# Optimization experiments

Hardware: AMD Instinct MI355X
Metric: run time of the kernel (lower is better)

The kernel has to match this reference:

```python
import jax, jax.numpy as jnp
import numpy as np

ALPHA = 0.2  # LeakyReLU negative slope
NEG_INF = -9e15


def setup_inputs() -> dict:
    key = jax.random.key(0)
    k1, k2, k3, k4, k5 = jax.random.split(key, 5)
    B, N, D = 4, 4096, 256
    feat = jax.random.normal(k1, (B, N, D), dtype=jnp.float32)
    adj = jax.random.randint(k2, (B, N, N), 0, 2, dtype=jnp.int32)
    W = jax.random.normal(k3, (D, D), dtype=jnp.float32) * (1.414 / np.sqrt(D))
    a_1 = jax.random.normal(k4, (D, 1), dtype=jnp.float32) * 0.1
    a_2 = jax.random.normal(k5, (D, 1), dtype=jnp.float32) * 0.1
    return {"feat": feat, "adj": adj, "W": W, "a_1": a_1, "a_2": a_2}


def reference(feat, adj, W, a_1, a_2):
    # h: [B, N, D]
    h = jnp.matmul(feat, W)
    Ax = jnp.matmul(h, a_1)  # [B, N, 1]
    Ay = jnp.matmul(h, a_2)  # [B, N, 1]
    # logits[b, i, j] = Ax[b, j] + Ay[b, i]
    logits = jnp.swapaxes(Ax, 1, 2) + Ay  # [B, N, N]
    e = jax.nn.leaky_relu(logits, negative_slope=ALPHA)
    e = jnp.where(adj > 0, e, jnp.float32(NEG_INF))
    attention = jax.nn.softmax(e, axis=-1)  # dropout p=0.0 -> identity
    h_prime = jnp.matmul(attention, feat)  # [B, N, in_features]
    h_out = jnp.matmul(h_prime, W)  # [B, N, out_features]
    return jax.nn.elu(h_out)
```

## Files before the change

### kernel.cpp

```cpp
#include <hip/hip_runtime.h>

typedef __attribute__((ext_vector_type(8))) short short8;
typedef __attribute__((ext_vector_type(4))) float f32x4;
typedef __attribute__((ext_vector_type(4))) int i32x4;
typedef __attribute__((ext_vector_type(2))) unsigned u32x2;

#define LOG2E 1.44269504f

__device__ __forceinline__ short f2bf(float f) {
  unsigned u = __builtin_bit_cast(unsigned, f);
  u += 0x7fffu + ((u >> 16) & 1u);
  return (short)(u >> 16);
}

__global__ void gat_wvec(const float* __restrict__ W, const float* __restrict__ a1,
                         const float* __restrict__ a2, float* __restrict__ w1,
                         float* __restrict__ w2) {
  __shared__ float a1f[256], a2f[256];
  const int tid = threadIdx.x;
  a1f[tid] = a1[tid];
  a2f[tid] = a2[tid];
  __syncthreads();
  float s1 = 0.f, s2 = 0.f;
  const float4* wr = (const float4*)(W + (size_t)tid * 256);
  for (int d0 = 0; d0 < 64; ++d0) {
    float4 v = wr[d0];
    s1 += v.x * a1f[d0 * 4] + v.y * a1f[d0 * 4 + 1] + v.z * a1f[d0 * 4 + 2] + v.w * a1f[d0 * 4 + 3];
    s2 += v.x * a2f[d0 * 4] + v.y * a2f[d0 * 4 + 1] + v.z * a2f[d0 * 4 + 2] + v.w * a2f[d0 * 4 + 3];
  }
  w1[tid] = s1;
  w2[tid] = s2;
}

__global__ void packB(const float* __restrict__ src, short* __restrict__ dst, int F) {
  const int tid = threadIdx.x;
  const int f = blockIdx.x, b = blockIdx.y;
  const int g = tid >> 4, l15 = tid & 15;
  const float* s = src + ((size_t)b * F * 32 + f * 32) * 256 + g * 16 + l15;
  short* d = dst + (((size_t)(b * F + f) * 16 + g) * 64) * 8;
#pragma unroll
  for (int q = 0; q < 4; ++q) {
    short8 v;
#pragma unroll
    for (int j8 = 0; j8 < 8; ++j8) v[j8] = f2bf(s[(q * 8 + j8) * 256]);
    *(short8*)(d + (q * 16 + l15) * 8) = v;
  }
}

__global__ void gat_axay(const float* __restrict__ feat, const float* __restrict__ w1,
                         const float* __restrict__ w2, float* __restrict__ AxL,
                         float* __restrict__ AyL) {
  const int lane = threadIdx.x & 63;
  const int row = blockIdx.x * 4 + (threadIdx.x >> 6);
  float4 fv = *(const float4*)(feat + (size_t)row * 256 + lane * 4);
  const float4 w1v = *(const float4*)(w1 + lane * 4);
  const float4 w2v = *(const float4*)(w2 + lane * 4);
  float s1 = fv.x * w1v.x + fv.y * w1v.y + fv.z * w1v.z + fv.w * w1v.w;
  float s2 = fv.x * w2v.x + fv.y * w2v.y + fv.z * w2v.z + fv.w * w2v.w;
#pragma unroll
  for (int off = 32; off >= 1; off >>= 1) {
    s1 += __shfl_xor(s1, off);
    s2 += __shfl_xor(s2, off);
  }
  if (lane == 0) { AxL[row] = s1 * LOG2E; AyL[row] = s2 * LOG2E; }
}

__global__ void gat_max(const float* __restrict__ AxL, float* __restrict__ MbL) {
  __shared__ float red[256];
  const int b = blockIdx.x, tid = threadIdx.x;
  float m = -3.4e38f;
  for (int i = tid; i < 4096; i += 256) m = fmaxf(m, AxL[b * 4096 + i]);
  red[tid] = m;
  __syncthreads();
  for (int s = 128; s > 0; s >>= 1) {
    if (tid < s) red[tid] = fmaxf(red[tid], red[tid + s]);
    __syncthreads();
  }
  if (tid == 0) MbL[b] = red[0];
}

__global__ __launch_bounds__(512, 4) void gat_attn(
    const short* __restrict__ featB,
    const int* __restrict__ adj,
    const float* __restrict__ AxL, const float* __restrict__ AyL,
    const float* __restrict__ MbL,
    const short* __restrict__ WB,
    float* __restrict__ out)
{
  __shared__ short smem[16896];

  const int tid = threadIdx.x;
  const int blk = blockIdx.x;
  const int x = blk & 7;
  const int b = x >> 1;
  const int it = ((blk >> 3) << 1) | (x & 1);
  const int i0 = it << 5;
  const int scoff = (blk >> 3) & 15;

  const int lane = tid & 63;
  const int aw = tid >> 6;

  float aLk[4], ddk[4];
#pragma unroll
  for (int k = 0; k < 4; ++k) {
    float ayL = AyL[b * 4096 + i0 + aw * 4 + k];
    float sL = ayL + MbL[b];
    float mrL = fmaxf(sL, 0.2f * sL);
    aLk[k] = ayL - mrL;
    ddk[k] = -0.8f * mrL;
  }
  const int* adjr = adj + ((size_t)(b * 4096 + i0 + aw * 4)) * 4096 + lane * 4;
  const float4* axp = (const float4*)(AxL + b * 4096) + lane;

  const int w = aw;
  const int rowg = (w & 1) << 4;
  const int cgrp = (w >> 1) << 2;
  const int l15 = lane & 15;
  const int q = lane >> 4;

  f32x4 acc[4], lac;
  lac = (f32x4){0.f, 0.f, 0.f, 0.f};
#pragma unroll
  for (int j = 0; j < 4; ++j) acc[j] = (f32x4){0.f, 0.f, 0.f, 0.f};

  short8 ones;
#pragma unroll
  for (int j = 0; j < 8; ++j) ones[j] = (short)0x3F80;

  const short* fbb = featB + (size_t)b * 128 * 16 * 64 * 8 + lane * 8;

  i32x4 adv[4];
  float4 axv;
  {
    const int w0 = scoff;
#pragma unroll
    for (int k = 0; k < 4; ++k)
      adv[k] = __builtin_nontemporal_load((const i32x4*)(adjr) + k * 1024 + w0 * 64);
    axv = axp[w0 * 64];
  }

  for (int sc = 0; sc < 16; ++sc) {
    const int wsc = (scoff + sc) & 15;
    const int pb = (sc & 1) * 8448;
    {
      const float* af = (const float*)&axv;
#pragma unroll
      for (int k = 0; k < 4; ++k) {
        unsigned pr[4];
#pragma unroll
        for (int u = 0; u < 4; ++u) {
          float v = af[u] + aLk[k];
          float uu = fmaxf(v, fmaf(0.2f, v, ddk[k]));
          unsigned ub = adv[k][u] > 0 ? __builtin_bit_cast(unsigned, uu) : 0xFF800000u;
          float p = __builtin_amdgcn_exp2f(__builtin_bit_cast(float, ub));
          pr[u] = __builtin_bit_cast(unsigned, p) + 0x8000u;
        }
        u32x2 pw;
        pw[0] = __builtin_amdgcn_perm(pr[1], pr[0], 0x07060302u);
        pw[1] = __builtin_amdgcn_perm(pr[3], pr[2], 0x07060302u);
        *(u32x2*)(smem + pb + (aw * 4 + k) * 264 + lane * 4) = pw;
      }
    }
    __syncthreads();

    if (sc < 15) {
      const int wn = (scoff + sc + 1) & 15;
#pragma unroll
      for (int k = 0; k < 4; ++k)
        adv[k] = __builtin_nontemporal_load((const i32x4*)(adjr) + k * 1024 + wn * 64);
      axv = axp[wn * 64];
    }

#pragma unroll
    for (int h = 0; h < 8; ++h) {
      const int f = wsc * 8 + h;
      const short* fb = fbb + (((size_t)f * 16 + cgrp) << 9);
      short8 a = *(const short8*)(smem + pb + (rowg + l15) * 264 + h * 32 + q * 8);
      lac = __builtin_amdgcn_mfma_f32_16x16x32_bf16(a, ones, lac, 0, 0, 0);
#pragma unroll
      for (int ct = 0; ct < 4; ++ct) {
        short8 bf = *(const short8*)(fb + (ct << 9));
        acc[ct] = __builtin_amdgcn_mfma_f32_16x16x32_bf16(a, bf, acc[ct], 0, 0, 0);
      }
    }
  }

  float linv[4];
#pragma unroll
  for (int reg = 0; reg < 4; ++reg) {
    float l = lac[reg];
    linv[reg] = l > 0.f ? 1.f / l : 0.f;
  }

  __syncthreads();
  short* hbuf = smem;
#pragma unroll
  for (int reg = 0; reg < 4; ++reg) {
    const int lr = rowg + q * 4 + reg;
#pragma unroll
    for (int ct = 0; ct < 4; ++ct)
      hbuf[lr * 264 + cgrp * 16 + ct * 16 + l15] = f2bf(acc[ct][reg] * linv[reg]);
  }
  __syncthreads();

  f32x4 ac2[4];
#pragma unroll
  for (int j = 0; j < 4; ++j) ac2[j] = (f32x4){0.f, 0.f, 0.f, 0.f};

  const short* wbb = WB + lane * 8;
#pragma unroll
  for (int f = 0; f < 8; ++f) {
    short8 a = *(const short8*)&hbuf[(rowg + l15) * 264 + f * 32 + q * 8];
    const short* wb = wbb + (((size_t)f * 16 + cgrp) << 9);
#pragma unroll
    for (int ct = 0; ct < 4; ++ct) {
      short8 bf = *(const short8*)(wb + (ct << 9));
      ac2[ct] = __builtin_amdgcn_mfma_f32_16x16x32_bf16(a, bf, ac2[ct], 0, 0, 0);
    }
  }

#pragma unroll
  for (int reg = 0; reg < 4; ++reg) {
    const int row = i0 + rowg + q * 4 + reg;
    float* orow = out + ((size_t)(b * 4096 + row)) * 256 + cgrp * 16 + l15;
#pragma unroll
    for (int ct = 0; ct < 4; ++ct) {
      float v = ac2[ct][reg];
      float o = v > 0.f ? v : (__builtin_amdgcn_exp2f(v * LOG2E) - 1.f);
      __builtin_nontemporal_store(o, orow + ct * 16);
    }
  }
}

extern "C" void kernel_launch(void* const* d_in, const int* in_sizes, int n_in,
                              void* d_out, int out_size, void* d_ws, size_t ws_size,
                              hipStream_t stream) {
  (void)in_sizes; (void)n_in; (void)out_size; (void)ws_size;
  const float* feat = (const float*)d_in[0];
  const int* adj = (const int*)d_in[1];
  const float* W = (const float*)d_in[2];
  const float* a1 = (const float*)d_in[3];
  const float* a2 = (const float*)d_in[4];
  float* out = (float*)d_out;

  char* ws = (char*)d_ws;
  short* featB   = (short*)ws;
  short* WB      = (short*)(ws + 8388608);
  float* AxL     = (float*)(ws + 8519680);
  float* AyL     = (float*)(ws + 8585216);
  float* MbL     = (float*)(ws + 8650752);
  float* w1      = (float*)(ws + 8651776);
  float* w2      = (float*)(ws + 8652800);

  hipLaunchKernelGGL(gat_wvec, dim3(1), dim3(256), 0, stream, W, a1, a2, w1, w2);
  hipLaunchKernelGGL(packB, dim3(8, 1), dim3(256), 0, stream, W, WB, 8);
  hipLaunchKernelGGL(packB, dim3(128, 4), dim3(256), 0, stream, feat, featB, 128);
  hipLaunchKernelGGL(gat_axay, dim3(4096), dim3(256), 0, stream, feat, w1, w2, AxL, AyL);
  hipLaunchKernelGGL(gat_max, dim3(4), dim3(256), 0, stream, AxL, MbL);
  hipLaunchKernelGGL(gat_attn, dim3(512), dim3(512), 0, stream, featB, adj, AxL, AyL, MbL, WB, out);
}
```

Baseline: 446.8 us.

## Fuse prologue kernels into one pass that reads feat once

Merges the W·a vector computation, the W and feat bf16 packing, and the Ax/Ay row dot products into a single prologue kernel. Feat is read once per 32-row tile and staged in shared memory for both the dot products and the bf16 repack, which removes three launches and a second read of feat. Every block now recomputes the 256x256 W·a product redundantly, adding about 512 blocks' worth of W reads and FLOPs. It also reorders the Ax load ahead of the adjacency loads in the attention kernel.

```diff
diff --git a/kernel.cpp b/kernel.cpp
--- a/kernel.cpp
+++ b/kernel.cpp
@@ -13,56 +13,84 @@
   return (short)(u >> 16);
 }
 
-__global__ void gat_wvec(const float* __restrict__ W, const float* __restrict__ a1,
-                         const float* __restrict__ a2, float* __restrict__ w1,
-                         float* __restrict__ w2) {
-  __shared__ float a1f[256], a2f[256];
+__global__ __launch_bounds__(256) void gat_pro(
+    const float* __restrict__ feat, const float* __restrict__ W,
+    const float* __restrict__ a1, const float* __restrict__ a2,
+    short* __restrict__ featB, short* __restrict__ WB,
+    float* __restrict__ AxL, float* __restrict__ AyL) {
+  __shared__ __align__(16) float a1f[256], a2f[256];
+  __shared__ __align__(16) float w1f[256], w2f[256];
+  __shared__ __align__(16) float tile[32][260];
   const int tid = threadIdx.x;
+  const int f = blockIdx.x, b = blockIdx.y;
+
   a1f[tid] = a1[tid];
   a2f[tid] = a2[tid];
   __syncthreads();
-  float s1 = 0.f, s2 = 0.f;
-  const float4* wr = (const float4*)(W + (size_t)tid * 256);
-  for (int d0 = 0; d0 < 64; ++d0) {
-    float4 v = wr[d0];
-    s1 += v.x * a1f[d0 * 4] + v.y * a1f[d0 * 4 + 1] + v.z * a1f[d0 * 4 + 2] + v.w * a1f[d0 * 4 + 3];
-    s2 += v.x * a2f[d0 * 4] + v.y * a2f[d0 * 4 + 1] + v.z * a2f[d0 * 4 + 2] + v.w * a2f[d0 * 4 + 3];
-  }
-  w1[tid] = s1;
-  w2[tid] = s2;
-}
-
-__global__ void packB(const float* __restrict__ src, short* __restrict__ dst, int F) {
-  const int tid = threadIdx.x;
-  const int f = blockIdx.x, b = blockIdx.y;
-  const int g = tid >> 4, l15 = tid & 15;
-  const float* s = src + ((size_t)b * F * 32 + f * 32) * 256 + g * 16 + l15;
-  short* d = dst + (((size_t)(b * F + f) * 16 + g) * 64) * 8;
-#pragma unroll
-  for (int q = 0; q < 4; ++q) {
-    short8 v;
-#pragma unroll
-    for (int j8 = 0; j8 < 8; ++j8) v[j8] = f2bf(s[(q * 8 + j8) * 256]);
-    *(short8*)(d + (q * 16 + l15) * 8) = v;
-  }
-}
-
-__global__ void gat_axay(const float* __restrict__ feat, const float* __restrict__ w1,
-                         const float* __restrict__ w2, float* __restrict__ AxL,
-                         float* __restrict__ AyL) {
-  const int lane = threadIdx.x & 63;
-  const int row = blockIdx.x * 4 + (threadIdx.x >> 6);
-  float4 fv = *(const float4*)(feat + (size_t)row * 256 + lane * 4);
-  const float4 w1v = *(const float4*)(w1 + lane * 4);
-  const float4 w2v = *(const float4*)(w2 + lane * 4);
-  float s1 = fv.x * w1v.x + fv.y * w1v.y + fv.z * w1v.z + fv.w * w1v.w;
-  float s2 = fv.x * w2v.x + fv.y * w2v.y + fv.z * w2v.z + fv.w * w2v.w;
-#pragma unroll
-  for (int off = 32; off >= 1; off >>= 1) {
-    s1 += __shfl_xor(s1, off);
-    s2 += __shfl_xor(s2, off);
-  }
-  if (lane == 0) { AxL[row] = s1 * LOG2E; AyL[row] = s2 * LOG2E; }
+
+  {
+    float s1 = 0.f, s2 = 0.f;
+    const float4* wr = (const float4*)(W + (size_t)tid * 256);
+    for (int d0 = 0; d0 < 64; ++d0) {
+      float4 v = wr[d0];
+      s1 += v.x * a1f[d0 * 4] + v.y * a1f[d0 * 4 + 1] + v.z * a1f[d0 * 4 + 2] + v.w * a1f[d0 * 4 + 3];
+      s2 += v.x * a2f[d0 * 4] + v.y * a2f[d0 * 4 + 1] + v.z * a2f[d0 * 4 + 2] + v.w * a2f[d0 * 4 + 3];
+    }
+    w1f[tid] = s1;
+    w2f[tid] = s2;
+  }
+  __syncthreads();
+
+  {
+    const int r = tid >> 3, g8 = tid & 7;
+    const float* frow = feat + ((size_t)(b * 4096 + f * 32 + r)) * 256;
+    float s1 = 0.f, s2 = 0.f;
+#pragma unroll
+    for (int k = 0; k < 8; ++k) {
+      const int c4 = g8 + 8 * k;
+      float4 v = *(const float4*)(frow + c4 * 4);
+      float4 u1 = *(const float4*)&w1f[c4 * 4];
+      float4 u2 = *(const float4*)&w2f[c4 * 4];
+      s1 += v.x * u1.x + v.y * u1.y + v.z * u1.z + v.w * u1.w;
+      s2 += v.x * u2.x + v.y * u2.y + v.z * u2.z + v.w * u2.w;
+      *(float4*)&tile[r][c4 * 4] = v;
+    }
+#pragma unroll
+    for (int off = 4; off >= 1; off >>= 1) {
+      s1 += __shfl_xor(s1, off);
+      s2 += __shfl_xor(s2, off);
+    }
+    if (g8 == 0) {
+      AxL[b * 4096 + f * 32 + r] = s1 * LOG2E;
+      AyL[b * 4096 + f * 32 + r] = s2 * LOG2E;
+    }
+  }
+  __syncthreads();
+
+  {
+    const int g = tid >> 4, l15 = tid & 15;
+    short* d = featB + (((size_t)((b * 128 + f) * 16 + g)) * 64) * 8;
+#pragma unroll
+    for (int q = 0; q < 4; ++q) {
+      short8 v;
+#pragma unroll
+      for (int j8 = 0; j8 < 8; ++j8) v[j8] = f2bf(tile[q * 8 + j8][g * 16 + l15]);
+      *(short8*)(d + (q * 16 + l15) * 8) = v;
+    }
+  }
+
+  if (b == 0 && f < 8) {
+    const int g = tid >> 4, l15 = tid & 15;
+    const float* s = W + ((size_t)f * 32) * 256 + g * 16 + l15;
+    short* d = WB + (((size_t)(f * 16 + g)) * 64) * 8;
+#pragma unroll
+    for (int q = 0; q < 4; ++q) {
+      short8 v;
+#pragma unroll
+      for (int j8 = 0; j8 < 8; ++j8) v[j8] = f2bf(s[(q * 8 + j8) * 256]);
+      *(short8*)(d + (q * 16 + l15) * 8) = v;
+    }
+  }
 }
 
 __global__ void gat_max(const float* __restrict__ AxL, float* __restrict__ MbL) {
@@ -133,10 +161,10 @@
   float4 axv;
   {
     const int w0 = scoff;
+    axv = axp[w0 * 64];
 #pragma unroll
     for (int k = 0; k < 4; ++k)
       adv[k] = __builtin_nontemporal_load((const i32x4*)(adjr) + k * 1024 + w0 * 64);
-    axv = axp[w0 * 64];
   }
 
   for (int sc = 0; sc < 16; ++sc) {
@@ -165,10 +193,10 @@
 
     if (sc < 15) {
       const int wn = (scoff + sc + 1) & 15;
+      axv = axp[wn * 64];
 #pragma unroll
       for (int k = 0; k < 4; ++k)
         adv[k] = __builtin_nontemporal_load((const i32x4*)(adjr) + k * 1024 + wn * 64);
-      axv = axp[wn * 64];
     }
 
 #pragma unroll
@@ -249,13 +277,9 @@
   float* AxL     = (float*)(ws + 8519680);
   float* AyL     = (float*)(ws + 8585216);
   float* MbL     = (float*)(ws + 8650752);
-  float* w1      = (float*)(ws + 8651776);
-  float* w2      = (float*)(ws + 8652800);
-
-  hipLaunchKernelGGL(gat_wvec, dim3(1), dim3(256), 0, stream, W, a1, a2, w1, w2);
-  hipLaunchKernelGGL(packB, dim3(8, 1), dim3(256), 0, stream, W, WB, 8);
-  hipLaunchKernelGGL(packB, dim3(128, 4), dim3(256), 0, stream, feat, featB, 128);
-  hipLaunchKernelGGL(gat_axay, dim3(4096), dim3(256), 0, stream, feat, w1, w2, AxL, AyL);
+  (void)ws_size;
+
+  hipLaunchKernelGGL(gat_pro, dim3(128, 4), dim3(256), 0, stream, feat, W, a1, a2, featB, WB, AxL, AyL);
   hipLaunchKernelGGL(gat_max, dim3(4), dim3(256), 0, stream, AxL, MbL);
   hipLaunchKernelGGL(gat_attn, dim3(512), dim3(512), 0, stream, featB, adj, AxL, AyL, MbL, WB, out);
 }
```

New measurement: 436.7 us. 1.02x faster.
